# Kernel tuning notes

Measured on AMD Instinct MI355X. Metric: run time of the kernel, lower is better.

Reference implementation:

```python
import jax, jax.numpy as jnp
import numpy as np

D_MODEL = 512
H = 8
DK = D_MODEL // H  # 64


def setup_inputs() -> dict:
    key = jax.random.key(0)
    ks = jax.random.split(key, 8)
    B, S = 2, 4096
    q = jax.random.normal(ks[0], (B, S, D_MODEL), dtype=jnp.float32)
    k = jax.random.normal(ks[1], (B, S, D_MODEL), dtype=jnp.float32)
    v = jax.random.normal(ks[2], (B, S, D_MODEL), dtype=jnp.float32)
    # per-head projection weights, torch nn.Linear layout [out, in], stacked over heads
    scale = 1.0 / np.sqrt(D_MODEL)
    Wq = jax.random.uniform(ks[3], (H, DK, D_MODEL), jnp.float32, -scale, scale)
    Wk = jax.random.uniform(ks[4], (H, DK, D_MODEL), jnp.float32, -scale, scale)
    Wv = jax.random.uniform(ks[5], (H, DK, D_MODEL), jnp.float32, -scale, scale)
    Wo = jax.random.uniform(ks[6], (D_MODEL, D_MODEL), jnp.float32, -scale, scale)
    # causal mask (True = keep), matches masked_fill(mask.logical_not(), -inf)
    mask = jnp.tril(jnp.ones((S, S), dtype=jnp.bool_))
    return {"q": q, "k": k, "v": v, "Wq": Wq, "Wk": Wk, "Wv": Wv, "Wo": Wo, "mask": mask}


def reference(q, k, v, Wq, Wk, Wv, Wo, mask):
    # per-head projections (stacked): x @ W^T for each head -> [B, H, S, DK]
    qh = jnp.einsum('bsd,hed->bhse', q, Wq)
    kh = jnp.einsum('bsd,hed->bhse', k, Wk)
    vh = jnp.einsum('bsd,hed->bhse', v, Wv)
    scaling = 1.0 / np.sqrt(DK)
    scores = jnp.einsum('bhse,bhte->bhst', qh, kh) * scaling  # [B,H,S,S]
    scores = jnp.where(mask, scores, -jnp.inf)
    attn = jax.nn.softmax(scores, axis=-1)
    heads = jnp.einsum('bhst,bhte->bhse', attn, vh)  # [B,H,S,DK]
    B, _, S, _ = heads.shape
    concat = jnp.transpose(heads, (0, 2, 1, 3)).reshape(B, S, D_MODEL)
    return concat @ Wo.T
```

## Files before the change

### kernel.cpp

```cpp
#include <hip/hip_runtime.h>
#include <hip/hip_bf16.h>
#include <math.h>

typedef __bf16 bf16_t;
typedef __bf16 bf16x8 __attribute__((ext_vector_type(8)));
typedef __bf16 bf16x4 __attribute__((ext_vector_type(4)));
typedef short short4v __attribute__((ext_vector_type(4)));
typedef float f32x4 __attribute__((ext_vector_type(4)));

__device__ __forceinline__ f32x4 mfma_k32(bf16x8 a, bf16x8 b, f32x4 c) {
    return __builtin_amdgcn_mfma_f32_16x16x32_bf16(a, b, c, 0, 0, 0);
}

__device__ __forceinline__ f32x4 mfma_k16(bf16x4 a, bf16x4 b, f32x4 c) {
#if __has_builtin(__builtin_amdgcn_mfma_f32_16x16x16_bf16)
    return __builtin_amdgcn_mfma_f32_16x16x16_bf16(a, b, c, 0, 0, 0);
#elif __has_builtin(__builtin_amdgcn_mfma_f32_16x16x16bf16_1k)
    short4v as, bs;
    __builtin_memcpy(&as, &a, 8);
    __builtin_memcpy(&bs, &b, 8);
    return __builtin_amdgcn_mfma_f32_16x16x16bf16_1k(as, bs, c, 0, 0, 0);
#else
    f32x4 d = c;
    asm volatile("v_mfma_f32_16x16x16_bf16 %0, %1, %2, %0" : "+v"(d) : "v"(a), "v"(b));
    return d;
#endif
}

__device__ __forceinline__ float fast_exp2(float x) {
#if __has_builtin(__builtin_amdgcn_exp2f)
    return __builtin_amdgcn_exp2f(x);
#else
    float r;
    asm("v_exp_f32 %0, %1" : "=v"(r) : "v"(x));
    return r;
#endif
}

__device__ __forceinline__ void async16(const bf16_t* g, __bf16* l) {
    __builtin_amdgcn_global_load_lds(
        (const __attribute__((address_space(1))) void*)g,
        (__attribute__((address_space(3))) void*)l, 16, 0, 0);
}

__device__ __forceinline__ int swz_col(int col, int row) {
    return (col & ~63) | ((((col >> 3) & 7) ^ (row & 7)) << 3) | (col & 7);
}

__device__ __forceinline__ bf16x8 cvt8(float4 a, float4 b) {
    bf16x8 w;
    w[0]=(__bf16)a.x; w[1]=(__bf16)a.y; w[2]=(__bf16)a.z; w[3]=(__bf16)a.w;
    w[4]=(__bf16)b.x; w[5]=(__bf16)b.y; w[6]=(__bf16)b.z; w[7]=(__bf16)b.w;
    return w;
}

__global__ __launch_bounds__(256) void cvt_W(const float* __restrict__ Wq,
                                             const float* __restrict__ Wk,
                                             const float* __restrict__ Wv,
                                             const float* __restrict__ Wo,
                                             bf16_t* __restrict__ Wc) {
    const int b2 = blockIdx.x;
    const int m = b2 >> 7;
    const float* src = m == 0 ? Wq : m == 1 ? Wk : m == 2 ? Wv : Wo;
    const float sc = (m == 0) ? 0.125f * 1.44269504088896f : 1.0f;
    size_t i = ((size_t)(b2 & 127) * 256 + threadIdx.x) * 8;
    int row = (int)(i >> 9), col = (int)(i & 511);
    float4 a0 = *(const float4*)(src + i), a1 = *(const float4*)(src + i + 4);
    bf16x8 o;
    o[0]=(__bf16)(a0.x*sc); o[1]=(__bf16)(a0.y*sc); o[2]=(__bf16)(a0.z*sc); o[3]=(__bf16)(a0.w*sc);
    o[4]=(__bf16)(a1.x*sc); o[5]=(__bf16)(a1.y*sc); o[6]=(__bf16)(a1.z*sc); o[7]=(__bf16)(a1.w*sc);
    *(bf16x8*)(Wc + (size_t)m * 262144 + (size_t)row * 512 + swz_col(col, row)) = o;
}

template<int F32>
__device__ __forceinline__ void stage64(__bf16* __restrict__ Sm,
                                        const bf16_t* __restrict__ Gb,
                                        const float* __restrict__ Gf,
                                        int row0, int kt,
                                        int wave, int r8, int c8, int lane) {
#pragma unroll
    for (int j = 0; j < 4; ++j) {
        const int rl = wave * 32 + j * 8 + r8;
        if (F32) {
            const float* s = Gf + (size_t)(row0 + rl) * 512 + kt + c8;
            float4 v0 = *(const float4*)s, v1 = *(const float4*)(s + 4);
            *(bf16x8*)&Sm[rl * 64 + (((lane & 7) ^ r8) << 3)] = cvt8(v0, v1);
        } else {
            async16(Gb + (size_t)(row0 + rl) * 512 + kt + c8,
                    &Sm[(wave * 32 + j * 8) * 64]);
        }
    }
}

template<int MODE, int AF32, int BF32>
__device__ __forceinline__ void gemm128_body(__bf16* __restrict__ Asm0,
                                             __bf16* __restrict__ Asm1,
                                             __bf16* __restrict__ Bsm0,
                                             __bf16* __restrict__ Bsm1,
                                             const bf16_t* __restrict__ Ab,
                                             const float* __restrict__ Af,
                                             const bf16_t* __restrict__ Bb,
                                             const float* __restrict__ Bf,
                                             void* __restrict__ outp,
                                             int m0, int n0) {
    const int tid  = threadIdx.x;
    const int wave = tid >> 6;
    const int lane = tid & 63;
    const int quad = lane >> 4;
    const int l16  = lane & 15;
    const int swz  = l16 & 7;
    const int r8 = lane >> 3;
    const int c8 = (lane & 7) * 8;
    const int mrow0 = (wave & 1) * 64;
    const int ncol0 = (wave >> 1) * 64;

    f32x4 acc[4][4];
    for (int i = 0; i < 4; ++i)
        for (int j = 0; j < 4; ++j) acc[i][j] = (f32x4){0.f, 0.f, 0.f, 0.f};

    for (int kt = 0; kt < 512; kt += 128) {
        __syncthreads();
        stage64<AF32>(Asm0, Ab, Af, m0, kt,      wave, r8, c8, lane);
        stage64<AF32>(Asm1, Ab, Af, m0, kt + 64, wave, r8, c8, lane);
        stage64<BF32>(Bsm0, Bb, Bf, n0, kt,      wave, r8, c8, lane);
        stage64<BF32>(Bsm1, Bb, Bf, n0, kt + 64, wave, r8, c8, lane);
        __syncthreads();

#pragma unroll
        for (int half = 0; half < 2; ++half) {
            const __bf16* As = half ? Asm1 : Asm0;
            const __bf16* Bs = half ? Bsm1 : Bsm0;
            for (int ks = 0; ks < 2; ++ks) {
                bf16x8 af[4];
                for (int mt = 0; mt < 4; ++mt)
                    af[mt] = *(const bf16x8*)&As[(mrow0 + mt * 16 + l16) * 64 + ((ks * 4 + quad) ^ swz) * 8];
                for (int nt = 0; nt < 4; ++nt) {
                    bf16x8 bf = *(const bf16x8*)&Bs[(ncol0 + nt * 16 + l16) * 64 + ((ks * 4 + quad) ^ swz) * 8];
                    for (int mt = 0; mt < 4; ++mt)
                        acc[mt][nt] = mfma_k32(af[mt], bf, acc[mt][nt]);
                }
            }
        }
    }

    if (MODE == 0) {
        bf16_t* out = (bf16_t*)outp;
        for (int nt = 0; nt < 4; ++nt) {
            int e = n0 + ncol0 + nt * 16 + l16;
            int h = e >> 6, el = e & 63;
            for (int mt = 0; mt < 4; ++mt)
                for (int r = 0; r < 4; ++r) {
                    int row = m0 + mrow0 + mt * 16 + quad * 4 + r;
                    int b = row >> 12, s = row & 4095;
                    int elp = (((el >> 3) ^ (row & 7)) << 3) | (el & 7);
                    out[(((size_t)(b * 8 + h)) * 4096 + s) * 64 + elp] = (bf16_t)acc[mt][nt][r];
                }
        }
    } else {
        bf16_t* out = (bf16_t*)outp;
        for (int nt = 0; nt < 4; ++nt) {
            int s_g = n0 + ncol0 + nt * 16 + l16;
            int b = s_g >> 12;
            int sbase = (s_g & 4095) & ~63;
            int f = 16 * ((l16 >> 2) & 3) + 4 * nt + (l16 & 3);
            for (int mt = 0; mt < 4; ++mt)
                for (int r = 0; r < 4; ++r) {
                    int e_g = m0 + mrow0 + mt * 16 + quad * 4 + r;
                    int h = e_g >> 6, el = e_g & 63;
                    int col = sbase | ((((f >> 3) ^ (e_g & 7)) & 7) << 3) | (f & 7);
                    out[(((size_t)(b * 8 + h)) * 64 + el) * 4096 + col] = (bf16_t)acc[mt][nt][r];
                }
        }
    }
}

__global__ __launch_bounds__(256) void proj_fused(const float* __restrict__ q,
                                                  const float* __restrict__ k,
                                                  const float* __restrict__ v,
                                                  const bf16_t* __restrict__ Wc,
                                                  bf16_t* __restrict__ qh,
                                                  bf16_t* __restrict__ kh,
                                                  bf16_t* __restrict__ vh) {
    __shared__ __bf16 Asm[2][128 * 64];
    __shared__ __bf16 Bsm[2][128 * 64];
    const int f = blockIdx.x;
    const int y = (f >> 3) & 3;
    const int x = (f & 7) | ((f >> 5) << 3);
    const int z = blockIdx.z;
    const bf16_t* W = Wc + (size_t)z * 262144;
    if (z == 0)
        gemm128_body<0, 1, 0>(Asm[0], Asm[1], Bsm[0], Bsm[1], nullptr, q, W, nullptr, qh, x * 128, y * 128);
    else if (z == 1)
        gemm128_body<0, 1, 0>(Asm[0], Asm[1], Bsm[0], Bsm[1], nullptr, k, W, nullptr, kh, x * 128, y * 128);
    else
        gemm128_body<1, 0, 1>(Asm[0], Asm[1], Bsm[0], Bsm[1], W, nullptr, nullptr, v, vh, y * 128, x * 128);
}

__global__ __launch_bounds__(256) void gemm_final(const bf16_t* __restrict__ Op,
                                                  const float* __restrict__ Lp,
                                                  const bf16_t* __restrict__ B,
                                                  float* __restrict__ out) {
    __shared__ __bf16 Asm[64 * 64];
    __shared__ __bf16 Bsm[64 * 64];
    const int fb = blockIdx.x;
    const int yb = (fb >> 3) & 7;
    const int xb = (fb & 7) | ((fb >> 6) << 3);
    const int m0 = xb * 64;
    const int n0 = yb * 64;
    const int tid  = threadIdx.x;
    const int wave = tid >> 6;
    const int lane = tid & 63;
    const int quad = lane >> 4;
    const int l16  = lane & 15;
    const int swz  = l16 & 7;
    const int r8 = lane >> 3;
    const int c8 = (lane & 7) * 8;
    const int mrow0 = (wave & 1) * 32;
    const int ncol0 = (wave >> 1) * 32;

    f32x4 acc[2][2];
    for (int i = 0; i < 2; ++i)
        for (int j = 0; j < 2; ++j) acc[i][j] = (f32x4){0.f, 0.f, 0.f, 0.f};

    for (int kt = 0; kt < 512; kt += 64) {
        const int h = kt >> 6;
        __syncthreads();
        for (int j = 0; j < 2; ++j)
            async16(B + (size_t)(n0 + wave * 16 + j * 8 + r8) * 512 + kt + c8,
                    &Bsm[(wave * 16 + j * 8) * 64]);
        for (int j = 0; j < 2; ++j) {
            const int rl  = wave * 16 + j * 8 + r8;
            const int row = m0 + rl;
            const int b   = row >> 12, sp = row & 4095;
            const size_t lidx = (size_t)(b * 8 + h) * 4096 + sp;
            bf16x8 a0 = *(const bf16x8*)(Op + lidx * 64 + c8);
            bf16x8 a1 = *(const bf16x8*)(Op + 4194304 + lidx * 64 + c8);
            float inv = 1.0f / (Lp[lidx] + Lp[65536 + lidx]);
            bf16x8 w;
            for (int i = 0; i < 8; ++i)
                w[i] = (bf16_t)(((float)a0[i] + (float)a1[i]) * inv);
            *(bf16x8*)&Asm[rl * 64 + (((lane & 7) ^ r8) << 3)] = w;
        }
        __syncthreads();

        for (int ks = 0; ks < 2; ++ks) {
            bf16x8 af[2];
            for (int mt = 0; mt < 2; ++mt)
                af[mt] = *(const bf16x8*)&Asm[(mrow0 + mt * 16 + l16) * 64 + ((ks * 4 + quad) ^ swz) * 8];
            for (int nt = 0; nt < 2; ++nt) {
                bf16x8 bf = *(const bf16x8*)&Bsm[(ncol0 + nt * 16 + l16) * 64 + ((ks * 4 + quad) ^ swz) * 8];
                for (int mt = 0; mt < 2; ++mt)
                    acc[mt][nt] = mfma_k32(af[mt], bf, acc[mt][nt]);
            }
        }
    }

    for (int nt = 0; nt < 2; ++nt) {
        int n = n0 + ncol0 + nt * 16 + l16;
        for (int mt = 0; mt < 2; ++mt)
            for (int r = 0; r < 4; ++r) {
                int row = m0 + mrow0 + mt * 16 + quad * 4 + r;
                out[(size_t)row * 512 + n] = acc[mt][nt][r];
            }
    }
}

__global__ __launch_bounds__(256, 4) void attn_kernel(const bf16_t* __restrict__ qh,
                                                      const bf16_t* __restrict__ kh,
                                                      const bf16_t* __restrict__ vh,
                                                      bf16_t* __restrict__ Opart,
                                                      float* __restrict__ Lpart) {
    __shared__ __bf16 SM[16384];
    __bf16* KSM = &SM[0];
    __bf16* VSM = &SM[8192];
    float* Osc = (float*)SM;
    float* Lsc = (float*)&SM[8320];

    const int id   = blockIdx.x;
    const int bh   = ((id & 7) << 1) | ((id >> 3) & 1);
    const int pair = (id >> 4) & 31;
    const int z    = (id >> 9) & 1;

    const int tid  = threadIdx.x;
    const int wave = tid >> 6;
    const int g2   = wave >> 1;
    const int wl   = wave & 1;
    const int lane = tid & 63;
    const int quad = lane >> 4;
    const int l16  = lane & 15;
    const int swz  = l16 & 7;
    const size_t base = (size_t)bh * 4096 * 64;
    const int r8 = lane >> 3;
    const int c8 = (lane & 7) * 8;

    bf16_t* Op = Opart + (size_t)z * 4194304;
    float*  Lp = Lpart + z * 65536;

    for (int leg = 0; leg < 2; ++leg) {
        const int qt = leg ? (63 - pair) : pair;
        const int q0 = qt * 64;

        bf16x8 qf[2][2];
        for (int g = 0; g < 2; ++g) {
            const bf16_t* qp = qh + base + (size_t)(q0 + wl * 32 + g * 16 + l16) * 64;
            qf[g][0] = *(const bf16x8*)(qp + ((quad ^ swz) * 8));
            qf[g][1] = *(const bf16x8*)(qp + (((4 + quad) ^ swz) * 8));
        }

        f32x4 o[2][4];
        for (int g = 0; g < 2; ++g)
            for (int i = 0; i < 4; ++i) o[g][i] = (f32x4){0.f, 0.f, 0.f, 0.f};
        float lsum[2] = {0.f, 0.f};

        const int S  = (qt + 2) >> 1;
        const int Sh = (S + 1) >> 1;
        const int it0 = z ? Sh : 0;
        const int it1 = z ? S : Sh;

        for (int it = it0; it < it1; ++it) {
            const int j0 = it * 128;
            __syncthreads();
            for (int p = 0; p < 2; ++p)
                for (int j = 0; j < 2; ++j) {
                    int row = wave * 16 + j * 8 + r8;
                    async16(kh + base + (size_t)(j0 + p * 64 + row) * 64 + c8,
                            KSM + (p * 64 + wave * 16 + j * 8) * 64);
                    async16(vh + (size_t)(bh * 64 + row) * 4096 + j0 + p * 64 + c8,
                            VSM + (p * 64 + wave * 16 + j * 8) * 64);
                }
            __syncthreads();

            const int pp = g2;
            const int koff = j0 + pp * 64 - q0;
            if (koff > wl * 32 + 31) continue;

            f32x4 st[2][4];
            for (int nt = 0; nt < 4; ++nt) {
                const __bf16* kr = KSM + (pp * 64 + nt * 16 + l16) * 64;
                bf16x8 kf0 = *(const bf16x8*)(kr + ((quad ^ swz) * 8));
                bf16x8 kf1 = *(const bf16x8*)(kr + (((4 + quad) ^ swz) * 8));
                for (int g = 0; g < 2; ++g) {
                    f32x4 zz = (f32x4){0.f, 0.f, 0.f, 0.f};
                    zz = mfma_k32(kf0, qf[g][0], zz);
                    zz = mfma_k32(kf1, qf[g][1], zz);
                    st[g][nt] = zz;
                }
            }

            bf16x4 pf[2][4];
            for (int g = 0; g < 2; ++g) {
                const int qb = wl * 32 + g * 16;
                if (koff + 63 <= qb) {
                    for (int nt = 0; nt < 4; ++nt)
                        for (int r = 0; r < 4; ++r) {
                            float p = fast_exp2(st[g][nt][r]);
                            lsum[g] += p;
                            pf[g][nt][r] = (bf16_t)p;
                        }
                } else {
                    const int qrow = qb + l16;
                    for (int nt = 0; nt < 4; ++nt)
                        for (int r = 0; r < 4; ++r) {
                            int key = nt * 16 + quad * 4 + r;
                            float p = (key + koff <= qrow) ? fast_exp2(st[g][nt][r]) : 0.f;
                            lsum[g] += p;
                            pf[g][nt][r] = (bf16_t)p;
                        }
                }
            }

            for (int dt = 0; dt < 4; ++dt)
                for (int kt2 = 0; kt2 < 2; ++kt2) {
                    bf16x8 vf = *(const bf16x8*)&VSM[(pp * 64 + dt * 16 + l16) * 64 + (((2 * quad + kt2) ^ swz) * 8)];
                    bf16x4 vlo = {vf[0], vf[1], vf[2], vf[3]};
                    bf16x4 vhi = {vf[4], vf[5], vf[6], vf[7]};
                    for (int g = 0; g < 2; ++g) {
                        o[g][dt] = mfma_k16(pf[g][2 * kt2], vlo, o[g][dt]);
                        o[g][dt] = mfma_k16(pf[g][2 * kt2 + 1], vhi, o[g][dt]);
                    }
                }
        }

        __syncthreads();
        if (g2 == 1) {
            for (int g = 0; g < 2; ++g) {
                float ls = lsum[g];
                ls += __shfl_xor(ls, 16);
                ls += __shfl_xor(ls, 32);
                const int qb = wl * 32 + g * 16;
                Lsc[qb + l16] = ls;
                for (int dt = 0; dt < 4; ++dt)
                    for (int r = 0; r < 4; ++r)
                        Osc[(qb + quad * 4 + r) * 65 + dt * 16 + l16] = o[g][dt][r];
            }
        }
        __syncthreads();
        if (g2 == 0) {
            for (int g = 0; g < 2; ++g) {
                float ls = lsum[g];
                ls += __shfl_xor(ls, 16);
                ls += __shfl_xor(ls, 32);
                const int qb = wl * 32 + g * 16;
                ls += Lsc[qb + l16];
                Lsc[qb + l16] = ls;
                for (int dt = 0; dt < 4; ++dt)
                    for (int r = 0; r < 4; ++r) {
                        int idx = (qb + quad * 4 + r) * 65 + dt * 16 + l16;
                        Osc[idx] = o[g][dt][r] + Osc[idx];
                    }
            }
        }
        __syncthreads();
        {
            const int q  = tid >> 2;
            const int e0 = (tid & 3) * 16;
            bf16x8 w0, w1;
            for (int i = 0; i < 8; ++i) {
                w0[i] = (bf16_t)Osc[q * 65 + e0 + i];
                w1[i] = (bf16_t)Osc[q * 65 + e0 + 8 + i];
            }
            size_t slot = ((size_t)(bh * 64 + qt)) * 4096 + q * 64 + e0;
            *(bf16x8*)&Op[slot]     = w0;
            *(bf16x8*)&Op[slot + 8] = w1;
            if (tid < 64) Lp[(bh * 64 + qt) * 64 + tid] = Lsc[tid];
        }
    }
}

extern "C" void kernel_launch(void* const* d_in, const int* in_sizes, int n_in,
                              void* d_out, int out_size, void* d_ws, size_t ws_size,
                              hipStream_t stream) {
    const float* q  = (const float*)d_in[0];
    const float* k  = (const float*)d_in[1];
    const float* v  = (const float*)d_in[2];
    const float* Wq = (const float*)d_in[3];
    const float* Wk = (const float*)d_in[4];
    const float* Wv = (const float*)d_in[5];
    const float* Wo = (const float*)d_in[6];
    float* out = (float*)d_out;

    bf16_t* ws = (bf16_t*)d_ws;
    const size_t R = (size_t)8192 * 512;
    bf16_t* opart = ws + R;
    bf16_t* vh = ws + 3 * R;
    bf16_t* Wc = ws + 4 * R;
    float*  Lp = (float*)(ws + 4 * R + 1048576);
    bf16_t* qh = (bf16_t*)d_out;
    bf16_t* kh = (bf16_t*)d_out + R;

    cvt_W<<<dim3(512), dim3(256), 0, stream>>>(Wq, Wk, Wv, Wo, Wc);
    proj_fused<<<dim3(256, 1, 3), dim3(256), 0, stream>>>(q, k, v, Wc, qh, kh, vh);
    attn_kernel<<<dim3(1024), dim3(256), 0, stream>>>(qh, kh, vh, opart, Lp);
    gemm_final<<<dim3(1024), dim3(256), 0, stream>>>(opart, Lp, Wc + 3 * 262144, out);
}
```

Measured before the change: 230.6 us.

## Prefetch fp32 operand tiles into registers and deepen K-step in output GEMM

In the projection GEMM, the fp32 operand for the next 128-wide K tile is loaded into registers ahead of time and overlaps with the MFMA work on the current tile. The bf16 operand still uses async copies into LDS. The final output GEMM now stages two 64-wide K slices per iteration with doubled LDS buffers, which halves the number of barrier pairs. This costs more registers, which may lower occupancy, and more LDS in the final GEMM.

```diff
diff --git a/kernel.cpp b/kernel.cpp
--- a/kernel.cpp
+++ b/kernel.cpp
@@ -70,26 +70,6 @@
     o[0]=(__bf16)(a0.x*sc); o[1]=(__bf16)(a0.y*sc); o[2]=(__bf16)(a0.z*sc); o[3]=(__bf16)(a0.w*sc);
     o[4]=(__bf16)(a1.x*sc); o[5]=(__bf16)(a1.y*sc); o[6]=(__bf16)(a1.z*sc); o[7]=(__bf16)(a1.w*sc);
     *(bf16x8*)(Wc + (size_t)m * 262144 + (size_t)row * 512 + swz_col(col, row)) = o;
-}
-
-template<int F32>
-__device__ __forceinline__ void stage64(__bf16* __restrict__ Sm,
-                                        const bf16_t* __restrict__ Gb,
-                                        const float* __restrict__ Gf,
-                                        int row0, int kt,
-                                        int wave, int r8, int c8, int lane) {
-#pragma unroll
-    for (int j = 0; j < 4; ++j) {
-        const int rl = wave * 32 + j * 8 + r8;
-        if (F32) {
-            const float* s = Gf + (size_t)(row0 + rl) * 512 + kt + c8;
-            float4 v0 = *(const float4*)s, v1 = *(const float4*)(s + 4);
-            *(bf16x8*)&Sm[rl * 64 + (((lane & 7) ^ r8) << 3)] = cvt8(v0, v1);
-        } else {
-            async16(Gb + (size_t)(row0 + rl) * 512 + kt + c8,
-                    &Sm[(wave * 32 + j * 8) * 64]);
-        }
-    }
 }
 
 template<int MODE, int AF32, int BF32>
@@ -113,18 +93,69 @@
     const int c8 = (lane & 7) * 8;
     const int mrow0 = (wave & 1) * 64;
     const int ncol0 = (wave >> 1) * 64;
+    const int wswz = ((lane & 7) ^ r8) << 3;
+
+    const float* Gf = AF32 ? Af : Bf;
+    const int    prow0 = AF32 ? m0 : n0;
+    const bf16_t* Gb = AF32 ? Bb : Ab;
+    const int     brow0 = AF32 ? n0 : m0;
 
     f32x4 acc[4][4];
     for (int i = 0; i < 4; ++i)
         for (int j = 0; j < 4; ++j) acc[i][j] = (f32x4){0.f, 0.f, 0.f, 0.f};
 
+    float4 pre[8][2];
+#pragma unroll
+    for (int sub = 0; sub < 2; ++sub)
+#pragma unroll
+        for (int j = 0; j < 4; ++j) {
+            const int rl = wave * 32 + j * 8 + r8;
+            const float* s = Gf + (size_t)(prow0 + rl) * 512 + sub * 64 + c8;
+            pre[sub * 4 + j][0] = *(const float4*)s;
+            pre[sub * 4 + j][1] = *(const float4*)(s + 4);
+        }
+
     for (int kt = 0; kt < 512; kt += 128) {
         __syncthreads();
-        stage64<AF32>(Asm0, Ab, Af, m0, kt,      wave, r8, c8, lane);
-        stage64<AF32>(Asm1, Ab, Af, m0, kt + 64, wave, r8, c8, lane);
-        stage64<BF32>(Bsm0, Bb, Bf, n0, kt,      wave, r8, c8, lane);
-        stage64<BF32>(Bsm1, Bb, Bf, n0, kt + 64, wave, r8, c8, lane);
-        __syncthreads();
+        {
+            __bf16* F0 = AF32 ? Asm0 : Bsm0;
+            __bf16* F1 = AF32 ? Asm1 : Bsm1;
+#pragma unroll
+            for (int sub = 0; sub < 2; ++sub) {
+                __bf16* Fs = sub ? F1 : F0;
+#pragma unroll
+                for (int j = 0; j < 4; ++j) {
+                    const int rl = wave * 32 + j * 8 + r8;
+                    *(bf16x8*)&Fs[rl * 64 + wswz] = cvt8(pre[sub * 4 + j][0], pre[sub * 4 + j][1]);
+                }
+            }
+        }
+        {
+            __bf16* B0 = AF32 ? Bsm0 : Asm0;
+            __bf16* B1 = AF32 ? Bsm1 : Asm1;
+#pragma unroll
+            for (int sub = 0; sub < 2; ++sub) {
+                __bf16* Bs2 = sub ? B1 : B0;
+#pragma unroll
+                for (int j = 0; j < 4; ++j) {
+                    const int rl = wave * 32 + j * 8 + r8;
+                    async16(Gb + (size_t)(brow0 + rl) * 512 + kt + sub * 64 + c8,
+                            &Bs2[(wave * 32 + j * 8) * 64]);
+                }
+            }
+        }
+        __syncthreads();
+        if (kt < 384) {
+#pragma unroll
+            for (int sub = 0; sub < 2; ++sub)
+#pragma unroll
+                for (int j = 0; j < 4; ++j) {
+                    const int rl = wave * 32 + j * 8 + r8;
+                    const float* s = Gf + (size_t)(prow0 + rl) * 512 + (kt + 128) + sub * 64 + c8;
+                    pre[sub * 4 + j][0] = *(const float4*)s;
+                    pre[sub * 4 + j][1] = *(const float4*)(s + 4);
+                }
+        }
 
 #pragma unroll
         for (int half = 0; half < 2; ++half) {
@@ -200,8 +231,8 @@
                                                   const float* __restrict__ Lp,
                                                   const bf16_t* __restrict__ B,
                                                   float* __restrict__ out) {
-    __shared__ __bf16 Asm[64 * 64];
-    __shared__ __bf16 Bsm[64 * 64];
+    __shared__ __bf16 Asm[2][64 * 64];
+    __shared__ __bf16 Bsm[2][64 * 64];
     const int fb = blockIdx.x;
     const int yb = (fb >> 3) & 7;
     const int xb = (fb & 7) | ((fb >> 6) << 3);
@@ -217,40 +248,47 @@
     const int c8 = (lane & 7) * 8;
     const int mrow0 = (wave & 1) * 32;
     const int ncol0 = (wave >> 1) * 32;
+    const int wswz = ((lane & 7) ^ r8) << 3;
 
     f32x4 acc[2][2];
     for (int i = 0; i < 2; ++i)
         for (int j = 0; j < 2; ++j) acc[i][j] = (f32x4){0.f, 0.f, 0.f, 0.f};
 
-    for (int kt = 0; kt < 512; kt += 64) {
-        const int h = kt >> 6;
-        __syncthreads();
-        for (int j = 0; j < 2; ++j)
-            async16(B + (size_t)(n0 + wave * 16 + j * 8 + r8) * 512 + kt + c8,
-                    &Bsm[(wave * 16 + j * 8) * 64]);
-        for (int j = 0; j < 2; ++j) {
-            const int rl  = wave * 16 + j * 8 + r8;
-            const int row = m0 + rl;
-            const int b   = row >> 12, sp = row & 4095;
-            const size_t lidx = (size_t)(b * 8 + h) * 4096 + sp;
-            bf16x8 a0 = *(const bf16x8*)(Op + lidx * 64 + c8);
-            bf16x8 a1 = *(const bf16x8*)(Op + 4194304 + lidx * 64 + c8);
-            float inv = 1.0f / (Lp[lidx] + Lp[65536 + lidx]);
-            bf16x8 w;
-            for (int i = 0; i < 8; ++i)
-                w[i] = (bf16_t)(((float)a0[i] + (float)a1[i]) * inv);
-            *(bf16x8*)&Asm[rl * 64 + (((lane & 7) ^ r8) << 3)] = w;
-        }
-        __syncthreads();
-
-        for (int ks = 0; ks < 2; ++ks) {
-            bf16x8 af[2];
-            for (int mt = 0; mt < 2; ++mt)
-                af[mt] = *(const bf16x8*)&Asm[(mrow0 + mt * 16 + l16) * 64 + ((ks * 4 + quad) ^ swz) * 8];
-            for (int nt = 0; nt < 2; ++nt) {
-                bf16x8 bf = *(const bf16x8*)&Bsm[(ncol0 + nt * 16 + l16) * 64 + ((ks * 4 + quad) ^ swz) * 8];
+    for (int kt = 0; kt < 512; kt += 128) {
+        __syncthreads();
+#pragma unroll
+        for (int half = 0; half < 2; ++half) {
+            const int h = (kt >> 6) + half;
+            for (int j = 0; j < 2; ++j)
+                async16(B + (size_t)(n0 + wave * 16 + j * 8 + r8) * 512 + kt + half * 64 + c8,
+                        &Bsm[half][(wave * 16 + j * 8) * 64]);
+            for (int j = 0; j < 2; ++j) {
+                const int rl  = wave * 16 + j * 8 + r8;
+                const int row = m0 + rl;
+                const int b   = row >> 12, sp = row & 4095;
+                const size_t lidx = (size_t)(b * 8 + h) * 4096 + sp;
+                bf16x8 a0 = *(const bf16x8*)(Op + lidx * 64 + c8);
+                bf16x8 a1 = *(const bf16x8*)(Op + 4194304 + lidx * 64 + c8);
+                float inv = 1.0f / (Lp[lidx] + Lp[65536 + lidx]);
+                bf16x8 w;
+                for (int i = 0; i < 8; ++i)
+                    w[i] = (bf16_t)(((float)a0[i] + (float)a1[i]) * inv);
+                *(bf16x8*)&Asm[half][rl * 64 + wswz] = w;
+            }
+        }
+        __syncthreads();
+
+#pragma unroll
+        for (int half = 0; half < 2; ++half) {
+            for (int ks = 0; ks < 2; ++ks) {
+                bf16x8 af[2];
                 for (int mt = 0; mt < 2; ++mt)
-                    acc[mt][nt] = mfma_k32(af[mt], bf, acc[mt][nt]);
+                    af[mt] = *(const bf16x8*)&Asm[half][(mrow0 + mt * 16 + l16) * 64 + ((ks * 4 + quad) ^ swz) * 8];
+                for (int nt = 0; nt < 2; ++nt) {
+                    bf16x8 bf = *(const bf16x8*)&Bsm[half][(ncol0 + nt * 16 + l16) * 64 + ((ks * 4 + quad) ^ swz) * 8];
+                    for (int mt = 0; mt < 2; ++mt)
+                        acc[mt][nt] = mfma_k32(af[mt], bf, acc[mt][nt]);
+                }
             }
         }
     }
```

After: 230.1 us. Within noise of the previous version (-0.2%).
